# Kernel tuning notes

Hardware: AMD Instinct MI355X
Metric: run time of the kernel (lower is better)

Reference implementation:

```python
import jax, jax.numpy as jnp
import numpy as np
import math

D_K = 64
ROUNDS = 4
BUCKET_LEN = 64


def _l2norm(x, axis):
    n = jnp.sqrt(jnp.sum(x * x, axis=axis, keepdims=True))
    return x / jnp.maximum(n, 1e-12)


def _look_back(x):
    # x: (B, n_buckets, bucket_len, ...) -> (B, n_buckets, 2*bucket_len, ...)
    # each bucket is concatenated with the previous bucket (wrapping at 0)
    shift = jnp.concatenate([x[:, -1:], x[:, :-1]], axis=1)
    return jnp.concatenate([shift, x], axis=2)


def _lsh_hash(query, rand_matrix):
    # returns position-tagged hashes: bucket_id * L + position, shape (B, L, R)
    B, L, D = query.shape
    qn = _l2norm(query, -1)
    rm = _l2norm(rand_matrix, 1)  # normalize over d_k dim, as in torch code
    xR = jnp.einsum('bld,bdrn->blrn', qn, rm)
    h = jnp.argmax(jnp.concatenate([xR, -xR], axis=-1), axis=-1).astype(jnp.int32)
    return h * L + jnp.arange(L, dtype=jnp.int32)[None, :, None]


def _attend(query, value, hash_indice, original_indice, sorted_hashes):
    B, L, D = query.shape
    nb = L // BUCKET_LEN
    R = ROUNDS
    # gather queries into hash-sorted order, per round: (B, L, D, R)
    rq = jnp.take_along_axis(query[:, :, :, None], hash_indice[:, :, None, :], axis=1)
    rq = rq.reshape(B, nb, BUCKET_LEN, D, R)
    lk = _l2norm(_look_back(rq), -2)  # keys = normalized lookback queries (shared QK)
    qk = jnp.einsum('bnijk,bnljk->bnilk', rq, lk) / math.sqrt(D_K)  # (B,nb,bl,2bl,R)
    # mask cross-bucket pairs
    sh = (sorted_hashes // L).reshape(B, nb, BUCKET_LEN, R)
    qk = jnp.where(sh[..., None, :] != _look_back(sh)[..., None, :, :], -1e9, qk)
    # mask self-attention (causal=False so no causal mask)
    qi = hash_indice.reshape(B, nb, BUCKET_LEN, R).astype(jnp.int32)
    ki = _look_back(qi)
    qk = jnp.where(qi[..., None, :] == ki[..., None, :, :], -1e5, qk)
    qk = qk.reshape(B, L, 2 * BUCKET_LEN, R)
    lse = jax.scipy.special.logsumexp(qk, axis=2)  # (B, L, R)
    p = jnp.exp(qk - lse[:, :, None, :]).reshape(B, nb, BUCKET_LEN, 2 * BUCKET_LEN, R)
    # gather values into sorted order and apply lookback attention
    rv = jnp.take_along_axis(value[:, :, :, None], hash_indice[:, :, None, :], axis=1)
    rv = rv.reshape(B, nb, BUCKET_LEN, D, R)
    att = jnp.einsum('bnijl,bnjkl->bnikl', p, _look_back(rv)).reshape(B, L, D, R)
    # scatter back to original order
    att = jnp.take_along_axis(att, original_indice[:, :, None, :], axis=1)
    lse = jnp.take_along_axis(lse, original_indice, axis=1)
    # NOTE: faithful to source, softmax over dim=1 (sequence dim)
    w = jax.nn.softmax(lse, axis=1)  # (B, L, R)
    return jnp.einsum('blir,blr->bli', att, w)  # (B, L, D)


def setup_inputs() -> dict:
    key = jax.random.key(0)
    k1, k2, k3 = jax.random.split(key, 3)
    B, L, D = 16, 8192, D_K
    n_buckets = L // BUCKET_LEN
    return {
        'query': jax.random.normal(k1, (B, L, D), jnp.float32),
        'value': jax.random.normal(k2, (B, L, D), jnp.float32),
        'rand_matrix': jax.random.normal(k3, (B, D, ROUNDS, n_buckets // 2), jnp.float32),
    }


def reference(query, value, rand_matrix):
    hashes = _lsh_hash(query, rand_matrix)          # (B, L, R) int32
    hash_indice = jnp.argsort(hashes, axis=1)       # sort positions by hash
    sorted_hashes = jnp.take_along_axis(hashes, hash_indice, axis=1)
    original_indice = jnp.argsort(hash_indice, axis=1)  # inverse permutation
    return _attend(query, value, hash_indice.astype(jnp.int32),
                   original_indice.astype(jnp.int32), sorted_hashes)
```

## Files before the change

### kernel.cpp

```cpp
#include <hip/hip_runtime.h>
#include <math.h>

#define B_   16
#define L_   8192
#define D_   64
#define R_   4
#define NB_  128
#define NH_  64

typedef float v2f __attribute__((ext_vector_type(2)));

__device__ __forceinline__ float dpp_xor1(float x) {
    return __int_as_float(__builtin_amdgcn_mov_dpp(__float_as_int(x), 0xB1, 0xf, 0xf, true));
}
__device__ __forceinline__ float dpp_xor2(float x) {
    return __int_as_float(__builtin_amdgcn_mov_dpp(__float_as_int(x), 0x4E, 0xf, 0xf, true));
}
__device__ __forceinline__ float quad_bcast0(float x) {
    return __int_as_float(__builtin_amdgcn_mov_dpp(__float_as_int(x), 0x00, 0xf, 0xf, true));
}
__device__ __forceinline__ float quad_bcast1(float x) {
    return __int_as_float(__builtin_amdgcn_mov_dpp(__float_as_int(x), 0x55, 0xf, 0xf, true));
}
__device__ __forceinline__ float quad_bcast2(float x) {
    return __int_as_float(__builtin_amdgcn_mov_dpp(__float_as_int(x), 0xAA, 0xf, 0xf, true));
}
__device__ __forceinline__ float quad_bcast3(float x) {
    return __int_as_float(__builtin_amdgcn_mov_dpp(__float_as_int(x), 0xFF, 0xf, 0xf, true));
}

#define VMCNT8 asm volatile("s_waitcnt vmcnt(8)" ::: "memory")
#define VMCNT4 asm volatile("s_waitcnt vmcnt(4)" ::: "memory")
#define VMCNT0 asm volatile("s_waitcnt vmcnt(0)" ::: "memory")
#define LGKM0  asm volatile("s_waitcnt lgkmcnt(0)" ::: "memory")

__device__ __forceinline__ void gl_lds16(const float* g, float* l) {
    __builtin_amdgcn_global_load_lds((const __attribute__((address_space(1))) void*)g,
                                     (__attribute__((address_space(3))) void*)l, 16, 0, 0);
}

__global__ __launch_bounds__(64) void k_rmnorm(const float* __restrict__ rm, double* __restrict__ rmn) {
    int b = blockIdx.x >> 2, r = blockIdx.x & 3;
    int n = threadIdx.x;
    float v[D_];
    double ss = 0.0;
    #pragma unroll
    for (int d = 0; d < D_; ++d) {
        float f = rm[((size_t)(b * D_ + d) * R_ + r) * NH_ + n];
        v[d] = f;
        ss += (double)f * (double)f;
    }
    double nrm = sqrt(ss); if (nrm < 1e-12) nrm = 1e-12;
    double inv = 1.0 / nrm;
    double* o = rmn + ((size_t)(b * R_ + r) * NH_ + n) * D_;
    #pragma unroll
    for (int d = 0; d < D_; ++d) o[d] = (double)v[d] * inv;
}

__global__ __launch_bounds__(256) void k_hash(const float* __restrict__ q, const double* __restrict__ rmn,
                                              float* __restrict__ rn, int* __restrict__ h) {
    __shared__ float rms[NH_ * D_];
    int b = blockIdx.z, r = blockIdx.y;
    int l = blockIdx.x * 256 + threadIdx.x;
    const double* src = rmn + (size_t)(b * R_ + r) * NH_ * D_;
    for (int i = threadIdx.x; i < NH_ * D_; i += 256) rms[i] = (float)src[i];
    const float* qp = q + ((size_t)b * L_ + l) * D_;
    v2f qv2[D_ / 2];
    double ss = 0.0;
    #pragma unroll
    for (int d = 0; d < D_; d += 4) {
        float4 f = *(const float4*)(qp + d);
        qv2[d >> 1]       = (v2f){f.x, f.y};
        qv2[(d >> 1) + 1] = (v2f){f.z, f.w};
        ss += (double)f.x * f.x + (double)f.y * f.y + (double)f.z * f.z + (double)f.w * f.w;
    }
    __syncthreads();
    float best = -1.0e30f, second = -1.0e30f; int bi = 0;
    for (int n = 0; n < NH_; ++n) {
        const float* kp = &rms[n * D_];
        v2f a0 = (v2f){0.f, 0.f}, a1 = a0;
        #pragma unroll
        for (int d = 0; d < D_; d += 4) {
            float4 kk = *(const float4*)(kp + d);
            a0 = __builtin_elementwise_fma(qv2[d >> 1],       (v2f){kk.x, kk.y}, a0);
            a1 = __builtin_elementwise_fma(qv2[(d >> 1) + 1], (v2f){kk.z, kk.w}, a1);
        }
        float s = (a0.x + a0.y) + (a1.x + a1.y);
        if (s > best)       { second = best; best = s; bi = n; }
        else if (s > second)  second = s;
        float ns = -s;
        if (ns > best)      { second = best; best = ns; bi = n + NH_; }
        else if (ns > second) second = ns;
    }
    float qn = (float)sqrt(ss);
    if (best - second < 1.2e-5f * qn + 1.0e-7f) {
        double bestd = -1.0e300; bi = 0;
        for (int n = 0; n < NH_; ++n) {
            const double* kp = src + n * D_;
            double a0 = 0, a1 = 0, a2 = 0, a3 = 0;
            #pragma unroll
            for (int d = 0; d < D_; d += 4) {
                a0 = fma((double)qv2[d >> 1].x,       kp[d],     a0);
                a1 = fma((double)qv2[d >> 1].y,       kp[d + 1], a1);
                a2 = fma((double)qv2[(d >> 1) + 1].x, kp[d + 2], a2);
                a3 = fma((double)qv2[(d >> 1) + 1].y, kp[d + 3], a3);
            }
            double s = (a0 + a1) + (a2 + a3);
            if (s > bestd)  { bestd = s;  bi = n; }
            if (-s > bestd) { bestd = -s; bi = n + NH_; }
        }
    }
    h[(size_t)(b * R_ + r) * L_ + l] = bi;
    if (r == 0) {
        double nrm = sqrt(ss); if (nrm < 1e-12) nrm = 1e-12;
        rn[(size_t)b * L_ + l] = (float)(1.0 / nrm);
    }
}

__global__ __launch_bounds__(256) void k_sort(const int* __restrict__ h, int* __restrict__ idx,
                                              int* __restrict__ sb, int* __restrict__ iv) {
    __shared__ unsigned int cnt[NB_ * 257];
    __shared__ unsigned int wsum[4];
    int br = blockIdx.x;
    const int* hh = h + (size_t)br * L_;
    int t = threadIdx.x;
    for (int i = t; i < NB_ * 257; i += 256) cnt[i] = 0;
    __syncthreads();
    int base = t * 32;
    for (int i = 0; i < 32; ++i) { int bk = hh[base + i]; cnt[bk * 257 + t]++; }
    __syncthreads();
    int fb = t * 128;
    unsigned int local = 0;
    for (int i = 0; i < 128; ++i) { unsigned g = fb + i; local += cnt[g + (g >> 8)]; }
    unsigned int v = local;
    #pragma unroll
    for (int off = 1; off < 64; off <<= 1) {
        unsigned int u = __shfl_up(v, off);
        if ((t & 63) >= off) v += u;
    }
    if ((t & 63) == 63) wsum[t >> 6] = v;
    __syncthreads();
    unsigned int wbase = 0;
    for (int w = 0; w < (t >> 6); ++w) wbase += wsum[w];
    unsigned int run = wbase + v - local;
    for (int i = 0; i < 128; ++i) {
        unsigned g = fb + i;
        unsigned int c0 = cnt[g + (g >> 8)];
        cnt[g + (g >> 8)] = run; run += c0;
    }
    __syncthreads();
    int* oi = idx + (size_t)br * L_;
    int* ob = sb  + (size_t)br * L_;
    int* ivp = iv + (size_t)br * L_;
    for (int i = 0; i < 32; ++i) {
        int l = base + i; int bk = hh[l];
        unsigned int pos = cnt[bk * 257 + t]++;
        oi[pos] = l; ob[pos] = bk; ivp[l] = (int)pos;
    }
}

__device__ __forceinline__ void issue_stage(const float* qb, const float* vb,
                                            const int4* krec, int kb16,
                                            float* kd, float* vd, int tid, int loadv) {
    #pragma unroll
    for (int t4 = 0; t4 < 4; ++t4) {
        int kl = krec[kb16 + t4 * 4 + (tid >> 4)].x;
        size_t off = (size_t)kl * D_ + (size_t)((tid & 15) * 4);
        gl_lds16(qb + off, kd + t4 * 256);
        if (loadv) gl_lds16(vb + off, vd + t4 * 256);
    }
}

__global__ __launch_bounds__(64) void k_flash(const float* __restrict__ q, const float* __restrict__ val,
                                              const int* __restrict__ idx, const int* __restrict__ sb,
                                              const float* __restrict__ rn, float* __restrict__ lse,
                                              const float* __restrict__ gm, const float* __restrict__ gs,
                                              float* __restrict__ out, float* __restrict__ contrib,
                                              int r_fixed, int omode) {
    __shared__ __align__(16) float kt[2][16 * 64];
    __shared__ __align__(16) float vt[2][16 * 64];
    __shared__ __align__(16) int4  krec[128];
    int tid = threadIdx.x;
    int c = blockIdx.x, b = blockIdx.z;
    int r = (r_fixed < 0) ? (int)blockIdx.y : r_fixed;
    size_t sbase = (size_t)(b * R_ + r) * L_;
    int cprev = (c + NB_ - 1) & (NB_ - 1);
    const float* qb = q   + (size_t)b * L_ * D_;
    const float* vb = val + (size_t)b * L_ * D_;
    int loadv = (omode != 2);
    for (int t = tid; t < 128; t += 64) {
        int pos = ((t < 64) ? cprev : c) * 64 + (t & 63);
        int kl = idx[sbase + pos];
        int kb = sb[sbase + pos];
        float kr = rn[(size_t)b * L_ + kl] * 0.125f;
        krec[t] = make_int4(kl, kb, __float_as_int(kr), 0);
    }
    int h = tid & 3;
    int posq = c * 64 + (tid >> 2) * 4;
    int mls[4];
    #pragma unroll
    for (int qq = 0; qq < 4; ++qq) mls[qq] = idx[sbase + posq + qq];
    int ownpos  = posq + h;
    int myl_own = idx[sbase + ownpos];
    int mybk_own = sb[sbase + ownpos];
    float m_own = 0.125f / rn[(size_t)b * L_ + myl_own];
    v2f qv2[4][8];
    #pragma unroll
    for (int qq = 0; qq < 4; ++qq) {
        const float* qp = qb + (size_t)mls[qq] * D_ + h * 16;
        #pragma unroll
        for (int i = 0; i < 16; i += 4) {
            float4 f = *(const float4*)(qp + i);
            qv2[qq][i >> 1]       = (v2f){f.x, f.y};
            qv2[qq][(i >> 1) + 1] = (v2f){f.z, f.w};
        }
    }
    float ps[4] = {0.0f, 0.0f, 0.0f, 0.0f};
    v2f acc2[4][8];
    #pragma unroll
    for (int qq = 0; qq < 4; ++qq)
        #pragma unroll
        for (int i = 0; i < 8; ++i) acc2[qq][i] = (v2f){0.0f, 0.0f};

    LGKM0;
    issue_stage(qb, vb, krec, 0, &kt[0][0], &vt[0][0], tid, loadv);

    #pragma unroll 1
    for (int s = 0; s < 8; ++s) {
        const float* ktp = &kt[s & 1][0];
        const float* vtp = &vt[s & 1][0];
        LGKM0;
        if (s < 7)
            issue_stage(qb, vb, krec, (s + 1) * 16, &kt[(s + 1) & 1][0], &vt[(s + 1) & 1][0], tid, loadv);
        if (s < 7) { if (loadv) { VMCNT8; } else { VMCNT4; } } else { VMCNT0; }
        __builtin_amdgcn_sched_barrier(0);
        for (int j = 0; j < 16; ++j) {
            int4 kv = krec[s * 16 + j];
            const float* kpj = ktp + j * 64 + h * 16;
            v2f a0 = (v2f){0.f, 0.f}, a1 = a0, a2 = a0, a3 = a0;
            #pragma unroll
            for (int i = 0; i < 16; i += 4) {
                float4 kk = *(const float4*)(kpj + i);
                v2f kA = (v2f){kk.x, kk.y}, kB = (v2f){kk.z, kk.w};
                int i2 = i >> 1;
                a0 = __builtin_elementwise_fma(qv2[0][i2], kA, a0);
                a0 = __builtin_elementwise_fma(qv2[0][i2 + 1], kB, a0);
                a1 = __builtin_elementwise_fma(qv2[1][i2], kA, a1);
                a1 = __builtin_elementwise_fma(qv2[1][i2 + 1], kB, a1);
                a2 = __builtin_elementwise_fma(qv2[2][i2], kA, a2);
                a2 = __builtin_elementwise_fma(qv2[2][i2 + 1], kB, a2);
                a3 = __builtin_elementwise_fma(qv2[3][i2], kA, a3);
                a3 = __builtin_elementwise_fma(qv2[3][i2 + 1], kB, a3);
            }
            float p0 = a0.x + a0.y, p1 = a1.x + a1.y, p2 = a2.x + a2.y, p3 = a3.x + a3.y;
            bool b0 = (h & 1), b1 = (h & 2) != 0;
            float u0 = b0 ? p1 : p0;
            float t0 = b0 ? p0 : p1;
            u0 += dpp_xor1(t0);
            float u2 = b0 ? p3 : p2;
            float t2 = b0 ? p2 : p3;
            u2 += dpp_xor1(t2);
            float dot = b1 ? u2 : u0;
            float t3 = b1 ? u0 : u2;
            dot += dpp_xor2(t3);
            float sc = dot * __int_as_float(kv.z);
            sc = (kv.y == mybk_own) ? sc : -1.0e9f;
            if (kv.x == myl_own) sc = -1.0e5f;
            float p = __expf(sc - m_own);
            ps[j & 3] += p;
            if (omode != 2) {
                v2f P0 = (v2f){quad_bcast0(p), quad_bcast0(p)};
                v2f P1 = (v2f){quad_bcast1(p), quad_bcast1(p)};
                v2f P2 = (v2f){quad_bcast2(p), quad_bcast2(p)};
                v2f P3 = (v2f){quad_bcast3(p), quad_bcast3(p)};
                const float* vpj = vtp + j * 64 + h * 16;
                #pragma unroll
                for (int i = 0; i < 16; i += 4) {
                    float4 vv = *(const float4*)(vpj + i);
                    v2f vA = (v2f){vv.x, vv.y}, vB = (v2f){vv.z, vv.w};
                    int i2 = i >> 1;
                    acc2[0][i2]     = __builtin_elementwise_fma(P0, vA, acc2[0][i2]);
                    acc2[0][i2 + 1] = __builtin_elementwise_fma(P0, vB, acc2[0][i2 + 1]);
                    acc2[1][i2]     = __builtin_elementwise_fma(P1, vA, acc2[1][i2]);
                    acc2[1][i2 + 1] = __builtin_elementwise_fma(P1, vB, acc2[1][i2 + 1]);
                    acc2[2][i2]     = __builtin_elementwise_fma(P2, vA, acc2[2][i2]);
                    acc2[2][i2 + 1] = __builtin_elementwise_fma(P2, vB, acc2[2][i2 + 1]);
                    acc2[3][i2]     = __builtin_elementwise_fma(P3, vA, acc2[3][i2]);
                    acc2[3][i2 + 1] = __builtin_elementwise_fma(P3, vB, acc2[3][i2 + 1]);
                }
            }
        }
    }
    float sum = (ps[0] + ps[1]) + (ps[2] + ps[3]);
    float lse_own, inv_own;
    if (sum > 0.0f) { lse_own = m_own + logf(sum); inv_own = 1.0f / sum; }
    else            { lse_own = -3.0e38f;          inv_own = 0.0f; }
    if (omode != 3) lse[sbase + ownpos] = lse_own;
    if (omode == 0 || omode == 1) {
        float ivs[4];
        ivs[0] = quad_bcast0(inv_own); ivs[1] = quad_bcast1(inv_own);
        ivs[2] = quad_bcast2(inv_own); ivs[3] = quad_bcast3(inv_own);
        float* cbase = contrib + ((omode == 0) ? (size_t)(b * R_ + r) * L_ : (size_t)b * L_) * D_;
        #pragma unroll
        for (int qq = 0; qq < 4; ++qq) {
            float* cp = cbase + (size_t)(posq + qq) * D_ + h * 16;
            #pragma unroll
            for (int i = 0; i < 16; i += 4) {
                int i2 = i >> 1;
                float4 o;
                o.x = acc2[qq][i2].x * ivs[qq];     o.y = acc2[qq][i2].y * ivs[qq];
                o.z = acc2[qq][i2 + 1].x * ivs[qq]; o.w = acc2[qq][i2 + 1].y * ivs[qq];
                *(float4*)(cp + i) = o;
            }
        }
    } else if (omode == 3) {
        int brr = b * R_ + r;
        float gmv = gm[brr], gsv = gs[brr];
        float ls4[4], iv4[4];
        ls4[0] = quad_bcast0(lse_own); ls4[1] = quad_bcast1(lse_own);
        ls4[2] = quad_bcast2(lse_own); ls4[3] = quad_bcast3(lse_own);
        iv4[0] = quad_bcast0(inv_own); iv4[1] = quad_bcast1(inv_own);
        iv4[2] = quad_bcast2(inv_own); iv4[3] = quad_bcast3(inv_own);
        #pragma unroll
        for (int qq = 0; qq < 4; ++qq) {
            float wq = __expf(ls4[qq] - gmv) * gsv * iv4[qq];
            float* op = out + ((size_t)b * L_ + mls[qq]) * D_ + h * 16;
            #pragma unroll
            for (int i = 0; i < 8; ++i) {
                unsafeAtomicAdd(op + 2 * i,     wq * acc2[qq][i].x);
                unsafeAtomicAdd(op + 2 * i + 1, wq * acc2[qq][i].y);
            }
        }
    }
}

__global__ __launch_bounds__(256) void k_wred(const float* __restrict__ lse, float* __restrict__ gm,
                                              float* __restrict__ gs, int r_w) {
    __shared__ float  sm[4];
    __shared__ double sd[4];
    int br = (r_w < 0) ? (int)blockIdx.x : ((int)blockIdx.x * R_ + r_w);
    const float* x = lse + (size_t)br * L_;
    int t = threadIdx.x;
    float mx = -3.0e38f;
    for (int i = t; i < L_; i += 256) mx = fmaxf(mx, x[i]);
    #pragma unroll
    for (int o = 32; o; o >>= 1) mx = fmaxf(mx, __shfl_down(mx, o));
    if ((t & 63) == 0) sm[t >> 6] = mx;
    __syncthreads();
    mx = fmaxf(fmaxf(sm[0], sm[1]), fmaxf(sm[2], sm[3]));
    double s = 0.0;
    for (int i = t; i < L_; i += 256) s += exp((double)x[i] - (double)mx);
    #pragma unroll
    for (int o = 32; o; o >>= 1) s += __shfl_down(s, o);
    if ((t & 63) == 0) sd[t >> 6] = s;
    __syncthreads();
    if (t == 0) { gm[br] = mx; gs[br] = (float)(1.0 / (sd[0] + sd[1] + sd[2] + sd[3])); }
}

__global__ __launch_bounds__(256) void k_comb_full(const float* __restrict__ contrib,
                                                   const int* __restrict__ iv,
                                                   const float* __restrict__ lse,
                                                   const float* __restrict__ gm,
                                                   const float* __restrict__ gs,
                                                   float* __restrict__ out) {
    int gid = blockIdx.x * 256 + threadIdx.x;
    int row = gid >> 2;
    int ch  = (gid & 3) * 16;
    int b = row >> 13, l = row & (L_ - 1);
    float s[16];
    #pragma unroll
    for (int i = 0; i < 16; ++i) s[i] = 0.0f;
    #pragma unroll
    for (int r = 0; r < R_; ++r) {
        int brr = b * R_ + r;
        int pos = iv[(size_t)brr * L_ + l];
        float w = expf(lse[(size_t)brr * L_ + pos] - gm[brr]) * gs[brr];
        const float* cp = contrib + ((size_t)brr * L_ + pos) * D_ + ch;
        #pragma unroll
        for (int i = 0; i < 16; i += 4) {
            float4 f = *(const float4*)(cp + i);
            s[i]   = fmaf(w, f.x, s[i]);   s[i+1] = fmaf(w, f.y, s[i+1]);
            s[i+2] = fmaf(w, f.z, s[i+2]); s[i+3] = fmaf(w, f.w, s[i+3]);
        }
    }
    float* op = out + (size_t)row * D_ + ch;
    #pragma unroll
    for (int i = 0; i < 16; i += 4) {
        float4 o; o.x = s[i]; o.y = s[i+1]; o.z = s[i+2]; o.w = s[i+3];
        *(float4*)(op + i) = o;
    }
}

__global__ __launch_bounds__(256) void k_comb_add(const float* __restrict__ contrib,
                                                  const int* __restrict__ iv,
                                                  const float* __restrict__ lse,
                                                  const float* __restrict__ gm,
                                                  const float* __restrict__ gs,
                                                  float* __restrict__ out, int r) {
    int gid = blockIdx.x * 256 + threadIdx.x;
    int row = gid >> 2;
    int ch  = (gid & 3) * 16;
    int b = row >> 13, l = row & (L_ - 1);
    int brr = b * R_ + r;
    int pos = iv[(size_t)brr * L_ + l];
    float w = expf(lse[(size_t)brr * L_ + pos] - gm[brr]) * gs[brr];
    const float* cp = contrib + ((size_t)b * L_ + pos) * D_ + ch;
    float* op = out + (size_t)row * D_ + ch;
    #pragma unroll
    for (int i = 0; i < 16; i += 4) {
        float4 f = *(const float4*)(cp + i);
        float4 o = *(const float4*)(op + i);
        o.x = fmaf(w, f.x, o.x); o.y = fmaf(w, f.y, o.y);
        o.z = fmaf(w, f.z, o.z); o.w = fmaf(w, f.w, o.w);
        *(float4*)(op + i) = o;
    }
}

#define OFF_RMN     0u
#define OFF_RN      2097152u
#define OFF_H       2621440u
#define OFF_IDX     4718592u
#define OFF_SB      6815744u
#define OFF_LSE     8912896u
#define OFF_GM      11010048u
#define OFF_GS      11010304u
#define OFF_INV     11010560u
#define OFF_CONTRIB 13107712u
#define CONTRIB_FULL_BYTES  134217728ull
#define CONTRIB_SLICE_BYTES 33554432ull

extern "C" void kernel_launch(void* const* d_in, const int* in_sizes, int n_in,
                              void* d_out, int out_size, void* d_ws, size_t ws_size,
                              hipStream_t stream) {
    const float* q  = (const float*)d_in[0];
    const float* v  = (const float*)d_in[1];
    const float* rm = (const float*)d_in[2];
    float* out = (float*)d_out;
    char* ws = (char*)d_ws;
    double* rmn = (double*)(ws + OFF_RMN);
    float*  rn  = (float*)(ws + OFF_RN);
    int*    h   = (int*)(ws + OFF_H);
    int*    idx = (int*)(ws + OFF_IDX);
    int*    sb  = (int*)(ws + OFF_SB);
    float*  lse = (float*)(ws + OFF_LSE);
    float*  gm  = (float*)(ws + OFF_GM);
    float*  gs  = (float*)(ws + OFF_GS);
    int*    iv  = (int*)(ws + OFF_INV);
    float*  contrib = (float*)(ws + OFF_CONTRIB);

    int tierA = (ws_size >= (size_t)OFF_CONTRIB + CONTRIB_FULL_BYTES) ? 1 : 0;
    int tierB = (!tierA && ws_size >= (size_t)OFF_CONTRIB + CONTRIB_SLICE_BYTES) ? 1 : 0;

    hipLaunchKernelGGL(k_rmnorm, dim3(B_ * R_), dim3(64), 0, stream, rm, rmn);
    hipLaunchKernelGGL(k_hash, dim3(L_ / 256, R_, B_), dim3(256), 0, stream, q, rmn, rn, h);
    hipLaunchKernelGGL(k_sort, dim3(B_ * R_), dim3(256), 0, stream, h, idx, sb, iv);

    if (tierA) {
        hipLaunchKernelGGL(k_flash, dim3(NB_, R_, B_), dim3(64), 0, stream, q, v, idx, sb, rn,
                           lse, gm, gs, out, contrib, -1, 0);
        hipLaunchKernelGGL(k_wred, dim3(B_ * R_), dim3(256), 0, stream, lse, gm, gs, -1);
        hipLaunchKernelGGL(k_comb_full, dim3(B_ * L_ * 4 / 256), dim3(256), 0, stream,
                           contrib, iv, lse, gm, gs, out);
    } else if (tierB) {
        hipMemsetAsync(d_out, 0, (size_t)B_ * L_ * D_ * sizeof(float), stream);
        for (int r = 0; r < R_; ++r) {
            hipLaunchKernelGGL(k_flash, dim3(NB_, 1, B_), dim3(64), 0, stream, q, v, idx, sb, rn,
                               lse, gm, gs, out, contrib, r, 1);
            hipLaunchKernelGGL(k_wred, dim3(B_), dim3(256), 0, stream, lse, gm, gs, r);
            hipLaunchKernelGGL(k_comb_add, dim3(B_ * L_ * 4 / 256), dim3(256), 0, stream,
                               contrib, iv, lse, gm, gs, out, r);
        }
    } else {
        hipMemsetAsync(d_out, 0, (size_t)B_ * L_ * D_ * sizeof(float), stream);
        hipLaunchKernelGGL(k_flash, dim3(NB_, R_, B_), dim3(64), 0, stream, q, v, idx, sb, rn,
                           lse, gm, gs, out, contrib, -1, 2);
        hipLaunchKernelGGL(k_wred, dim3(B_ * R_), dim3(256), 0, stream, lse, gm, gs, -1);
        hipLaunchKernelGGL(k_flash, dim3(NB_, R_, B_), dim3(64), 0, stream, q, v, idx, sb, rn,
                           lse, gm, gs, out, contrib, -1, 3);
    }
}
```

Before: 561.1 us.

## Pack sorted index, bucket and norm into one record; load values directly

The sort kernel now writes one packed int2 record per sorted position, holding the position, bucket id in the high bits, and the reciprocal norm. The flash kernel reads these records straight from global memory instead of staging a krec table in LDS. V tiles are no longer staged through LDS; each thread loads its value slice with direct float4 global loads per key. Dropping the V LDS buffer and setting launch_bounds(64,2) reduces LDS use and aims at higher occupancy. The cost is uncoalesced, latency-exposed V loads inside the inner loop and repeated global record reads per key.

```diff
diff --git a/kernel.cpp b/kernel.cpp
--- a/kernel.cpp
+++ b/kernel.cpp
@@ -29,7 +29,6 @@
     return __int_as_float(__builtin_amdgcn_mov_dpp(__float_as_int(x), 0xFF, 0xf, 0xf, true));
 }
 
-#define VMCNT8 asm volatile("s_waitcnt vmcnt(8)" ::: "memory")
 #define VMCNT4 asm volatile("s_waitcnt vmcnt(4)" ::: "memory")
 #define VMCNT0 asm volatile("s_waitcnt vmcnt(0)" ::: "memory")
 #define LGKM0  asm volatile("s_waitcnt lgkmcnt(0)" ::: "memory")
@@ -117,12 +116,13 @@
     }
 }
 
-__global__ __launch_bounds__(256) void k_sort(const int* __restrict__ h, int* __restrict__ idx,
-                                              int* __restrict__ sb, int* __restrict__ iv) {
+__global__ __launch_bounds__(256) void k_sort(const int* __restrict__ h, const float* __restrict__ rn,
+                                              int* __restrict__ iv, int2* __restrict__ rec) {
     __shared__ unsigned int cnt[NB_ * 257];
     __shared__ unsigned int wsum[4];
     int br = blockIdx.x;
     const int* hh = h + (size_t)br * L_;
+    const float* rnb = rn + (size_t)(br >> 2) * L_;
     int t = threadIdx.x;
     for (int i = t; i < NB_ * 257; i += 256) cnt[i] = 0;
     __syncthreads();
@@ -149,61 +149,40 @@
         cnt[g + (g >> 8)] = run; run += c0;
     }
     __syncthreads();
-    int* oi = idx + (size_t)br * L_;
-    int* ob = sb  + (size_t)br * L_;
     int* ivp = iv + (size_t)br * L_;
+    int2* rp = rec + (size_t)br * L_;
     for (int i = 0; i < 32; ++i) {
         int l = base + i; int bk = hh[l];
         unsigned int pos = cnt[bk * 257 + t]++;
-        oi[pos] = l; ob[pos] = bk; ivp[l] = (int)pos;
-    }
-}
-
-__device__ __forceinline__ void issue_stage(const float* qb, const float* vb,
-                                            const int4* krec, int kb16,
-                                            float* kd, float* vd, int tid, int loadv) {
-    #pragma unroll
-    for (int t4 = 0; t4 < 4; ++t4) {
-        int kl = krec[kb16 + t4 * 4 + (tid >> 4)].x;
-        size_t off = (size_t)kl * D_ + (size_t)((tid & 15) * 4);
-        gl_lds16(qb + off, kd + t4 * 256);
-        if (loadv) gl_lds16(vb + off, vd + t4 * 256);
-    }
-}
-
-__global__ __launch_bounds__(64) void k_flash(const float* __restrict__ q, const float* __restrict__ val,
-                                              const int* __restrict__ idx, const int* __restrict__ sb,
-                                              const float* __restrict__ rn, float* __restrict__ lse,
-                                              const float* __restrict__ gm, const float* __restrict__ gs,
-                                              float* __restrict__ out, float* __restrict__ contrib,
-                                              int r_fixed, int omode) {
+        ivp[l] = (int)pos;
+        rp[pos] = make_int2(l | (bk << 16), __float_as_int(rnb[l]));
+    }
+}
+
+__global__ __launch_bounds__(64, 2) void k_flash(const float* __restrict__ q, const float* __restrict__ val,
+                                                 const int2* __restrict__ rec, float* __restrict__ lse,
+                                                 const float* __restrict__ gm, const float* __restrict__ gs,
+                                                 float* __restrict__ out, float* __restrict__ contrib,
+                                                 int r_fixed, int omode) {
     __shared__ __align__(16) float kt[2][16 * 64];
-    __shared__ __align__(16) float vt[2][16 * 64];
-    __shared__ __align__(16) int4  krec[128];
     int tid = threadIdx.x;
     int c = blockIdx.x, b = blockIdx.z;
     int r = (r_fixed < 0) ? (int)blockIdx.y : r_fixed;
     size_t sbase = (size_t)(b * R_ + r) * L_;
-    int cprev = (c + NB_ - 1) & (NB_ - 1);
+    const int2* recs = rec + sbase;
     const float* qb = q   + (size_t)b * L_ * D_;
     const float* vb = val + (size_t)b * L_ * D_;
     int loadv = (omode != 2);
-    for (int t = tid; t < 128; t += 64) {
-        int pos = ((t < 64) ? cprev : c) * 64 + (t & 63);
-        int kl = idx[sbase + pos];
-        int kb = sb[sbase + pos];
-        float kr = rn[(size_t)b * L_ + kl] * 0.125f;
-        krec[t] = make_int4(kl, kb, __float_as_int(kr), 0);
-    }
     int h = tid & 3;
     int posq = c * 64 + (tid >> 2) * 4;
+    int2 rown = recs[posq + h];
+    int own_w0 = rown.x;
+    int own_bk = own_w0 & 0xFFFF0000;
+    float m_own = 0.125f / __int_as_float(rown.y);
     int mls[4];
     #pragma unroll
-    for (int qq = 0; qq < 4; ++qq) mls[qq] = idx[sbase + posq + qq];
-    int ownpos  = posq + h;
-    int myl_own = idx[sbase + ownpos];
-    int mybk_own = sb[sbase + ownpos];
-    float m_own = 0.125f / rn[(size_t)b * L_ + myl_own];
+    for (int qq = 0; qq < 4; ++qq) mls[qq] = recs[posq + qq].x & 0xFFFF;
+    int ownpos = posq + h;
     v2f qv2[4][8];
     #pragma unroll
     for (int qq = 0; qq < 4; ++qq) {
@@ -222,20 +201,46 @@
         #pragma unroll
         for (int i = 0; i < 8; ++i) acc2[qq][i] = (v2f){0.0f, 0.0f};
 
-    LGKM0;
-    issue_stage(qb, vb, krec, 0, &kt[0][0], &vt[0][0], tid, loadv);
+    {
+        int ck0 = ((c + NB_ - 1) & (NB_ - 1)) * 64;
+        #pragma unroll
+        for (int t4 = 0; t4 < 4; ++t4) {
+            int kl = recs[ck0 + t4 * 4 + (tid >> 4)].x & 0xFFFF;
+            gl_lds16(qb + (size_t)kl * D_ + ((tid & 15) * 4), &kt[0][t4 * 256]);
+        }
+    }
 
     #pragma unroll 1
     for (int s = 0; s < 8; ++s) {
         const float* ktp = &kt[s & 1][0];
-        const float* vtp = &vt[s & 1][0];
         LGKM0;
-        if (s < 7)
-            issue_stage(qb, vb, krec, (s + 1) * 16, &kt[(s + 1) & 1][0], &vt[(s + 1) & 1][0], tid, loadv);
-        if (s < 7) { if (loadv) { VMCNT8; } else { VMCNT4; } } else { VMCNT0; }
+        if (s < 7) {
+            int sn = s + 1;
+            int ckn = ((c + NB_ - 1 + (sn >> 2)) & (NB_ - 1)) * 64 + (sn & 3) * 16;
+            float* dst = &kt[sn & 1][0];
+            #pragma unroll
+            for (int t4 = 0; t4 < 4; ++t4) {
+                int kl = recs[ckn + t4 * 4 + (tid >> 4)].x & 0xFFFF;
+                gl_lds16(qb + (size_t)kl * D_ + ((tid & 15) * 4), dst + t4 * 256);
+            }
+            VMCNT4;
+        } else {
+            VMCNT0;
+        }
         __builtin_amdgcn_sched_barrier(0);
+        int jb = ((c + NB_ - 1 + (s >> 2)) & (NB_ - 1)) * 64 + (s & 3) * 16;
         for (int j = 0; j < 16; ++j) {
-            int4 kv = krec[s * 16 + j];
+            int2 kv = recs[jb + j];
+            int skl = kv.x & 0xFFFF;
+            float skr = __int_as_float(kv.y) * 0.125f;
+            const float* vpj = vb + (size_t)skl * D_ + h * 16;
+            float4 vv0, vv1, vv2, vv3;
+            if (loadv) {
+                vv0 = *(const float4*)(vpj + 0);
+                vv1 = *(const float4*)(vpj + 4);
+                vv2 = *(const float4*)(vpj + 8);
+                vv3 = *(const float4*)(vpj + 12);
+            }
             const float* kpj = ktp + j * 64 + h * 16;
             v2f a0 = (v2f){0.f, 0.f}, a1 = a0, a2 = a0, a3 = a0;
             #pragma unroll
@@ -263,31 +268,52 @@
             float dot = b1 ? u2 : u0;
             float t3 = b1 ? u0 : u2;
             dot += dpp_xor2(t3);
-            float sc = dot * __int_as_float(kv.z);
-            sc = (kv.y == mybk_own) ? sc : -1.0e9f;
-            if (kv.x == myl_own) sc = -1.0e5f;
+            float sc = dot * skr;
+            sc = (own_bk == (kv.x & 0xFFFF0000)) ? sc : -1.0e9f;
+            if (own_w0 == kv.x) sc = -1.0e5f;
             float p = __expf(sc - m_own);
             ps[j & 3] += p;
-            if (omode != 2) {
+            if (loadv) {
                 v2f P0 = (v2f){quad_bcast0(p), quad_bcast0(p)};
                 v2f P1 = (v2f){quad_bcast1(p), quad_bcast1(p)};
                 v2f P2 = (v2f){quad_bcast2(p), quad_bcast2(p)};
                 v2f P3 = (v2f){quad_bcast3(p), quad_bcast3(p)};
-                const float* vpj = vtp + j * 64 + h * 16;
-                #pragma unroll
-                for (int i = 0; i < 16; i += 4) {
-                    float4 vv = *(const float4*)(vpj + i);
-                    v2f vA = (v2f){vv.x, vv.y}, vB = (v2f){vv.z, vv.w};
-                    int i2 = i >> 1;
-                    acc2[0][i2]     = __builtin_elementwise_fma(P0, vA, acc2[0][i2]);
-                    acc2[0][i2 + 1] = __builtin_elementwise_fma(P0, vB, acc2[0][i2 + 1]);
-                    acc2[1][i2]     = __builtin_elementwise_fma(P1, vA, acc2[1][i2]);
-                    acc2[1][i2 + 1] = __builtin_elementwise_fma(P1, vB, acc2[1][i2 + 1]);
-                    acc2[2][i2]     = __builtin_elementwise_fma(P2, vA, acc2[2][i2]);
-                    acc2[2][i2 + 1] = __builtin_elementwise_fma(P2, vB, acc2[2][i2 + 1]);
-                    acc2[3][i2]     = __builtin_elementwise_fma(P3, vA, acc2[3][i2]);
-                    acc2[3][i2 + 1] = __builtin_elementwise_fma(P3, vB, acc2[3][i2 + 1]);
-                }
+                v2f vA0 = (v2f){vv0.x, vv0.y}, vB0 = (v2f){vv0.z, vv0.w};
+                v2f vA1 = (v2f){vv1.x, vv1.y}, vB1 = (v2f){vv1.z, vv1.w};
+                v2f vA2 = (v2f){vv2.x, vv2.y}, vB2 = (v2f){vv2.z, vv2.w};
+                v2f vA3 = (v2f){vv3.x, vv3.y}, vB3 = (v2f){vv3.z, vv3.w};
+                acc2[0][0] = __builtin_elementwise_fma(P0, vA0, acc2[0][0]);
+                acc2[0][1] = __builtin_elementwise_fma(P0, vB0, acc2[0][1]);
+                acc2[0][2] = __builtin_elementwise_fma(P0, vA1, acc2[0][2]);
+                acc2[0][3] = __builtin_elementwise_fma(P0, vB1, acc2[0][3]);
+                acc2[0][4] = __builtin_elementwise_fma(P0, vA2, acc2[0][4]);
+                acc2[0][5] = __builtin_elementwise_fma(P0, vB2, acc2[0][5]);
+                acc2[0][6] = __builtin_elementwise_fma(P0, vA3, acc2[0][6]);
+                acc2[0][7] = __builtin_elementwise_fma(P0, vB3, acc2[0][7]);
+                acc2[1][0] = __builtin_elementwise_fma(P1, vA0, acc2[1][0]);
+                acc2[1][1] = __builtin_elementwise_fma(P1, vB0, acc2[1][1]);
+                acc2[1][2] = __builtin_elementwise_fma(P1, vA1, acc2[1][2]);
+                acc2[1][3] = __builtin_elementwise_fma(P1, vB1, acc2[1][3]);
+                acc2[1][4] = __builtin_elementwise_fma(P1, vA2, acc2[1][4]);
+                acc2[1][5] = __builtin_elementwise_fma(P1, vB2, acc2[1][5]);
+                acc2[1][6] = __builtin_elementwise_fma(P1, vA3, acc2[1][6]);
+                acc2[1][7] = __builtin_elementwise_fma(P1, vB3, acc2[1][7]);
+                acc2[2][0] = __builtin_elementwise_fma(P2, vA0, acc2[2][0]);
+                acc2[2][1] = __builtin_elementwise_fma(P2, vB0, acc2[2][1]);
+                acc2[2][2] = __builtin_elementwise_fma(P2, vA1, acc2[2][2]);
+                acc2[2][3] = __builtin_elementwise_fma(P2, vB1, acc2[2][3]);
+                acc2[2][4] = __builtin_elementwise_fma(P2, vA2, acc2[2][4]);
+                acc2[2][5] = __builtin_elementwise_fma(P2, vB2, acc2[2][5]);
+                acc2[2][6] = __builtin_elementwise_fma(P2, vA3, acc2[2][6]);
+                acc2[2][7] = __builtin_elementwise_fma(P2, vB3, acc2[2][7]);
+                acc2[3][0] = __builtin_elementwise_fma(P3, vA0, acc2[3][0]);
+                acc2[3][1] = __builtin_elementwise_fma(P3, vB0, acc2[3][1]);
+                acc2[3][2] = __builtin_elementwise_fma(P3, vA1, acc2[3][2]);
+                acc2[3][3] = __builtin_elementwise_fma(P3, vB1, acc2[3][3]);
+                acc2[3][4] = __builtin_elementwise_fma(P3, vA2, acc2[3][4]);
+                acc2[3][5] = __builtin_elementwise_fma(P3, vB2, acc2[3][5]);
+                acc2[3][6] = __builtin_elementwise_fma(P3, vA3, acc2[3][6]);
+                acc2[3][7] = __builtin_elementwise_fma(P3, vB3, acc2[3][7]);
             }
         }
     }
@@ -417,15 +443,14 @@
 }
 
 #define OFF_RMN     0u
-#define OFF_RN      2097152u
-#define OFF_H       2621440u
-#define OFF_IDX     4718592u
-#define OFF_SB      6815744u
-#define OFF_LSE     8912896u
-#define OFF_GM      11010048u
-#define OFF_GS      11010304u
-#define OFF_INV     11010560u
-#define OFF_CONTRIB 13107712u
+#define OFF_REC     0u
+#define OFF_RN      4194304u
+#define OFF_H       4718592u
+#define OFF_LSE     6815744u
+#define OFF_GM      8912896u
+#define OFF_GS      8913152u
+#define OFF_INV     8913408u
+#define OFF_CONTRIB 11010560u
 #define CONTRIB_FULL_BYTES  134217728ull
 #define CONTRIB_SLICE_BYTES 33554432ull
 
@@ -438,10 +463,9 @@
     float* out = (float*)d_out;
     char* ws = (char*)d_ws;
     double* rmn = (double*)(ws + OFF_RMN);
+    int2*   rec = (int2*)(ws + OFF_REC);
     float*  rn  = (float*)(ws + OFF_RN);
     int*    h   = (int*)(ws + OFF_H);
-    int*    idx = (int*)(ws + OFF_IDX);
-    int*    sb  = (int*)(ws + OFF_SB);
     float*  lse = (float*)(ws + OFF_LSE);
     float*  gm  = (float*)(ws + OFF_GM);
     float*  gs  = (float*)(ws + OFF_GS);
@@ -453,10 +477,10 @@
 
     hipLaunchKernelGGL(k_rmnorm, dim3(B_ * R_), dim3(64), 0, stream, rm, rmn);
     hipLaunchKernelGGL(k_hash, dim3(L_ / 256, R_, B_), dim3(256), 0, stream, q, rmn, rn, h);
-    hipLaunchKernelGGL(k_sort, dim3(B_ * R_), dim3(256), 0, stream, h, idx, sb, iv);
+    hipLaunchKernelGGL(k_sort, dim3(B_ * R_), dim3(256), 0, stream, h, rn, iv, rec);
 
     if (tierA) {
-        hipLaunchKernelGGL(k_flash, dim3(NB_, R_, B_), dim3(64), 0, stream, q, v, idx, sb, rn,
+        hipLaunchKernelGGL(k_flash, dim3(NB_, R_, B_), dim3(64), 0, stream, q, v, rec,
                            lse, gm, gs, out, contrib, -1, 0);
         hipLaunchKernelGGL(k_wred, dim3(B_ * R_), dim3(256), 0, stream, lse, gm, gs, -1);
         hipLaunchKernelGGL(k_comb_full, dim3(B_ * L_ * 4 / 256), dim3(256), 0, stream,
@@ -464,7 +488,7 @@
     } else if (tierB) {
         hipMemsetAsync(d_out, 0, (size_t)B_ * L_ * D_ * sizeof(float), stream);
         for (int r = 0; r < R_; ++r) {
-            hipLaunchKernelGGL(k_flash, dim3(NB_, 1, B_), dim3(64), 0, stream, q, v, idx, sb, rn,
+            hipLaunchKernelGGL(k_flash, dim3(NB_, 1, B_), dim3(64), 0, stream, q, v, rec,
                                lse, gm, gs, out, contrib, r, 1);
             hipLaunchKernelGGL(k_wred, dim3(B_), dim3(256), 0, stream, lse, gm, gs, r);
             hipLaunchKernelGGL(k_comb_add, dim3(B_ * L_ * 4 / 256), dim3(256), 0, stream,
@@ -472,10 +496,10 @@
         }
     } else {
         hipMemsetAsync(d_out, 0, (size_t)B_ * L_ * D_ * sizeof(float), stream);
-        hipLaunchKernelGGL(k_flash, dim3(NB_, R_, B_), dim3(64), 0, stream, q, v, idx, sb, rn,
+        hipLaunchKernelGGL(k_flash, dim3(NB_, R_, B_), dim3(64), 0, stream, q, v, rec,
                            lse, gm, gs, out, contrib, -1, 2);
         hipLaunchKernelGGL(k_wred, dim3(B_ * R_), dim3(256), 0, stream, lse, gm, gs, -1);
-        hipLaunchKernelGGL(k_flash, dim3(NB_, R_, B_), dim3(64), 0, stream, q, v, idx, sb, rn,
+        hipLaunchKernelGGL(k_flash, dim3(NB_, R_, B_), dim3(64), 0, stream, q, v, rec,
                            lse, gm, gs, out, contrib, -1, 3);
     }
 }
```

Result: slower. 689.9 us (+22.9%).
